# Optimization experiments

Hardware: AMD Instinct MI355X
Metric: run time of the kernel (lower is better)

Reference implementation:

```python
import jax, jax.numpy as jnp
import numpy as np

BATCH = 4096
DIM = 128
TEMP = 0.5
EPS = 1e-8


def _neg_mask(batch):
    n = 2 * batch
    m = np.ones((n, n), dtype=bool)
    np.fill_diagonal(m, False)
    idx = np.arange(batch)
    m[idx, idx + batch] = False
    m[idx + batch, idx] = False
    return m


def setup_inputs() -> dict:
    key = jax.random.key(0)
    k1, k2 = jax.random.split(key)
    zx = jax.random.normal(k1, (BATCH, DIM), dtype=jnp.float32)
    zy = jax.random.normal(k2, (BATCH, DIM), dtype=jnp.float32)
    return {"zx": zx, "zy": zy}


def reference(zx, zy):
    batch = zx.shape[0]
    n = 2 * batch  # N = 2 * batch_size
    z = jnp.concatenate([zx, zy], axis=0)  # [N, D]
    # cosine similarity = normalized GEMM (avoids O(N^2*D) intermediate)
    norm = jnp.maximum(jnp.linalg.norm(z, axis=1, keepdims=True), EPS)
    zn = z / norm
    sim = (zn @ zn.T) / TEMP  # [N, N]
    # positives: diagonals at offsets +batch and -batch
    sim_xy = jnp.diagonal(sim, offset=batch)
    sim_yx = jnp.diagonal(sim, offset=-batch)
    positives = jnp.concatenate([sim_xy, sim_yx]).reshape(n, 1)  # [N, 1]
    # negatives: mask out diagonal and positive pairs (static boolean mask)
    mask = _neg_mask(batch)
    negatives = sim[mask].reshape(n, n - 2)  # [N, N-2]
    logits = jnp.concatenate([positives, negatives], axis=1)  # [N, N-1]
    # CrossEntropy(labels=0, reduction='sum') / N
    loss = jnp.sum(jax.nn.logsumexp(logits, axis=1) - logits[:, 0]) / n
    return loss
```

## Files before the change

kernel.cpp:

```cpp
#include <hip/hip_runtime.h>
#include <hip/hip_bf16.h>

#define BATCH 4096
#define NROWS 8192
#define DIM   128
#define NTILE 64

typedef __bf16 bf16x8 __attribute__((ext_vector_type(8)));
typedef __bf16 bf16x2 __attribute__((ext_vector_type(2)));
typedef float  f32x4  __attribute__((ext_vector_type(4)));

typedef const __attribute__((address_space(1))) unsigned int* gptr_t;
typedef __attribute__((address_space(3))) unsigned int* lptr_t;

__global__ __launch_bounds__(256) void normalize_kernel(
    const float* __restrict__ zx, const float* __restrict__ zy,
    ushort* __restrict__ zn, float* __restrict__ S, float* __restrict__ out)
{
  const int tid  = threadIdx.x;
  const int lane = tid & 63;
  const int w    = tid >> 6;
  const int row  = blockIdx.x * 4 + w;
  if (blockIdx.x < 32) S[blockIdx.x * 256 + tid] = 0.f;
  if (blockIdx.x == 0 && tid == 0) out[0] = 0.f;
  const float* src = (row < BATCH) ? (zx + (size_t)row * DIM)
                                   : (zy + (size_t)(row - BATCH) * DIM);
  float2 v = ((const float2*)src)[lane];
  float ss = v.x * v.x + v.y * v.y;
#pragma unroll
  for (int off = 1; off < 64; off <<= 1)
    ss += __shfl_xor(ss, off, 64);
  float inv = 1.0f / fmaxf(sqrtf(ss), 1e-8f);
  bf16x2 st;
  st.x = (__bf16)(v.x * inv);
  st.y = (__bf16)(v.y * inv);
  reinterpret_cast<bf16x2*>(zn + (size_t)row * DIM)[lane] = st;
}

__global__ __launch_bounds__(256, 2) void simloss_kernel(
    const ushort* __restrict__ zn, float* __restrict__ S,
    float* __restrict__ P)
{
  __shared__ ushort Bs[2][128 * 128];
  const int tid  = threadIdx.x;
  const int lane = tid & 63;
  const int w    = tid >> 6;
  const int wr   = w >> 1, wc = w & 1;
  const int q    = lane >> 4;
  const int l15  = lane & 15;

  const int p  = blockIdx.x >> 4;
  const int ch = blockIdx.x & 15;
  const int o0 = (ch == 0) ? 0 : 1 + ch * 4;
  const int T  = (ch == 0) ? 5 : 4;
  const int L0 = p + 1;

  auto tile_rc = [&](int o, int& rb, int& cb) {
    if (o < L0) { rb = p;      cb = o; }
    else        { rb = 63 - p; cb = o - L0; }
  };

  auto stage = [&](int cb, int buf) {
    const int C0 = cb * 128;
#pragma unroll
    for (int j = 0; j < 8; ++j) {
      const int Lbase = w * 512 + j * 64;
      const int row   = w * 32 + j * 4 + q;
      const int c     = l15 ^ (row & 15);
      const ushort* g = zn + (size_t)(C0 + row) * DIM + c * 8;
      __builtin_amdgcn_global_load_lds((gptr_t)g, (lptr_t)(&Bs[buf][Lbase * 8]),
                                       16, 0, 0);
    }
  };

  bf16x8 af[4][4];
  auto loadA = [&](int rb) {
    const int arow = rb * 128 + wr * 64 + l15;
#pragma unroll
    for (int mi = 0; mi < 4; ++mi)
#pragma unroll
      for (int ks = 0; ks < 4; ++ks) {
        const ushort* ap = zn + (size_t)(arow + mi * 16) * DIM + ks * 32 + q * 8;
        af[mi][ks] = *reinterpret_cast<const bf16x8*>(ap);
      }
  };

  int rb0, cb0;
  tile_rc(o0, rb0, cb0);
  stage(cb0, 0);
  loadA(rb0);

  f32x4 Srow[4];
#pragma unroll
  for (int mi = 0; mi < 4; ++mi) Srow[mi] = (f32x4){0.f, 0.f, 0.f, 0.f};

  const float K1 = 2.8853900817779268f;

  __syncthreads();

  for (int t = 0; t < T; ++t) {
    const int o = o0 + t;
    int trb, tcb;
    tile_rc(o, trb, tcb);
    int nrb = -1, ncb = -1;
    if (t + 1 < T) {
      tile_rc(o + 1, nrb, ncb);
      stage(ncb, (t & 1) ^ 1);
    }

    const ushort* bsc = &Bs[t & 1][0];

    f32x4 acc[4][4];
#pragma unroll
    for (int mi = 0; mi < 4; ++mi)
#pragma unroll
      for (int ni = 0; ni < 4; ++ni)
        acc[mi][ni] = (f32x4){0.f, 0.f, 0.f, 0.f};

#pragma unroll
    for (int ks = 0; ks < 4; ++ks) {
      bf16x8 bf[4];
#pragma unroll
      for (int ni = 0; ni < 4; ++ni) {
        const int nl  = wc * 64 + ni * 16 + l15;
        const int ck  = ks * 4 + q;
        const int L   = nl * 16 + (ck ^ (nl & 15));
        bf[ni] = *reinterpret_cast<const bf16x8*>(bsc + L * 8);
      }
#pragma unroll
      for (int mi = 0; mi < 4; ++mi)
#pragma unroll
        for (int ni = 0; ni < 4; ++ni)
          acc[mi][ni] = __builtin_amdgcn_mfma_f32_16x16x32_bf16(
              af[mi][ks], bf[ni], acc[mi][ni], 0, 0, 0);
    }

    const bool diag = (trb == tcb);
    float Scol[4];
#pragma unroll
    for (int ni = 0; ni < 4; ++ni) Scol[ni] = 0.f;

#pragma unroll
    for (int mi = 0; mi < 4; ++mi)
#pragma unroll
      for (int ni = 0; ni < 4; ++ni) {
        f32x4 vv;
#pragma unroll
        for (int r = 0; r < 4; ++r) {
          float d = acc[mi][ni][r];
          float v = __builtin_amdgcn_exp2f(fmaf(d, K1, -K1));
          if (diag) {
            const int rl = wr * 64 + mi * 16 + q * 4 + r;
            const int cl = wc * 64 + ni * 16 + l15;
            if (rl == cl) v = 0.f;
          }
          vv[r] = v;
        }
        Srow[mi] += vv;
        Scol[ni] += (vv[0] + vv[1]) + (vv[2] + vv[3]);
      }

    if (trb - tcb == 32) {
#pragma unroll
      for (int mi = 0; mi < 4; ++mi) {
        const int rl0 = wr * 64 + mi * 16 + q * 4;
#pragma unroll
        for (int ni = 0; ni < 4; ++ni) {
          const int cl = wc * 64 + ni * 16 + l15;
#pragma unroll
          for (int r = 0; r < 4; ++r) {
            if (cl == rl0 + r) {
              const int gr = trb * 128 + rl0 + r;
              const float pv = 2.0f * acc[mi][ni][r];
              P[gr] = pv;
              P[gr - 4096] = pv;
            }
          }
        }
      }
    }

    if (!diag) {
#pragma unroll
      for (int ni = 0; ni < 4; ++ni) {
        float v = Scol[ni];
        v += __shfl_xor(v, 16, 64);
        v += __shfl_xor(v, 32, 64);
        if (lane < 16)
          atomicAdd(&S[tcb * 128 + wc * 64 + ni * 16 + l15], v);
      }
    }

    const bool flushR = (t == T - 1) || (nrb != trb);
    if (flushR) {
#pragma unroll
      for (int mi = 0; mi < 4; ++mi)
#pragma unroll
        for (int r = 0; r < 4; ++r) {
          float v = Srow[mi][r];
          v += __shfl_xor(v, 1, 64);
          v += __shfl_xor(v, 2, 64);
          v += __shfl_xor(v, 4, 64);
          v += __shfl_xor(v, 8, 64);
          if (l15 == 0)
            atomicAdd(&S[trb * 128 + wr * 64 + mi * 16 + q * 4 + r], v);
        }
#pragma unroll
      for (int mi = 0; mi < 4; ++mi) Srow[mi] = (f32x4){0.f, 0.f, 0.f, 0.f};
    }

    if (t + 1 < T) {
      if (nrb != trb) loadA(nrb);
      __syncthreads();
    }
  }
}

__global__ __launch_bounds__(256) void finalize_kernel(
    const float* __restrict__ S, const float* __restrict__ P,
    float* __restrict__ out)
{
  const int i = blockIdx.x * 256 + threadIdx.x;
  float c = 2.0f + logf(S[i]) - P[i];
#pragma unroll
  for (int off = 1; off < 64; off <<= 1)
    c += __shfl_xor(c, off, 64);
  __shared__ float wsum[4];
  const int lane = threadIdx.x & 63, w = threadIdx.x >> 6;
  if (lane == 0) wsum[w] = c;
  __syncthreads();
  if (threadIdx.x == 0)
    atomicAdd(out, (wsum[0] + wsum[1] + wsum[2] + wsum[3]) * (1.0f / NROWS));
}

extern "C" void kernel_launch(void* const* d_in, const int* in_sizes, int n_in,
                              void* d_out, int out_size, void* d_ws, size_t ws_size,
                              hipStream_t stream)
{
  const float* zx = (const float*)d_in[0];
  const float* zy = (const float*)d_in[1];
  ushort* zn = (ushort*)d_ws;
  float*  P  = (float*)((char*)d_ws + (size_t)NROWS * DIM * 2);
  float*  S  = P + NROWS;
  float*  out = (float*)d_out;

  normalize_kernel<<<NROWS / 4, 256, 0, stream>>>(zx, zy, zn, S, out);
  simloss_kernel<<<512, 256, 0, stream>>>(zn, S, P);
  finalize_kernel<<<NROWS / 256, 256, 0, stream>>>(S, P, out);
}
```

Before: 83.76 us.

## Drop LDS staging of B tiles, load B fragments directly from global, double grid

The simloss kernel no longer stages B tiles into shared memory with global_load_lds double buffering and barriers. Each wave now loads its B fragments straight from global memory (relying on L1/L2 caching), and the block-level syncthreads calls are removed. The grid doubles to 1024 blocks with 2-3 tiles each, and the occupancy hint rises to 3 blocks per SM. The aim is to remove LDS traffic and synchronisation and to improve latency hiding. The cost is redundant global/L2 loads across waves and less reuse of B per block.

```diff
diff --git a/kernel.cpp b/kernel.cpp
--- a/kernel.cpp
+++ b/kernel.cpp
@@ -9,9 +9,6 @@
 typedef __bf16 bf16x8 __attribute__((ext_vector_type(8)));
 typedef __bf16 bf16x2 __attribute__((ext_vector_type(2)));
 typedef float  f32x4  __attribute__((ext_vector_type(4)));
-
-typedef const __attribute__((address_space(1))) unsigned int* gptr_t;
-typedef __attribute__((address_space(3))) unsigned int* lptr_t;
 
 __global__ __launch_bounds__(256) void normalize_kernel(
     const float* __restrict__ zx, const float* __restrict__ zy,
@@ -37,11 +34,10 @@
   reinterpret_cast<bf16x2*>(zn + (size_t)row * DIM)[lane] = st;
 }
 
-__global__ __launch_bounds__(256, 2) void simloss_kernel(
+__global__ __launch_bounds__(256, 3) void simloss_kernel(
     const ushort* __restrict__ zn, float* __restrict__ S,
     float* __restrict__ P)
 {
-  __shared__ ushort Bs[2][128 * 128];
   const int tid  = threadIdx.x;
   const int lane = tid & 63;
   const int w    = tid >> 6;
@@ -49,10 +45,10 @@
   const int q    = lane >> 4;
   const int l15  = lane & 15;
 
-  const int p  = blockIdx.x >> 4;
-  const int ch = blockIdx.x & 15;
-  const int o0 = (ch == 0) ? 0 : 1 + ch * 4;
-  const int T  = (ch == 0) ? 5 : 4;
+  const int p  = blockIdx.x >> 5;
+  const int ch = blockIdx.x & 31;
+  const int o0 = (ch == 0) ? 0 : 1 + ch * 2;
+  const int T  = (ch == 0) ? 3 : 2;
   const int L0 = p + 1;
 
   auto tile_rc = [&](int o, int& rb, int& cb) {
@@ -60,19 +56,6 @@
     else        { rb = 63 - p; cb = o - L0; }
   };
 
-  auto stage = [&](int cb, int buf) {
-    const int C0 = cb * 128;
-#pragma unroll
-    for (int j = 0; j < 8; ++j) {
-      const int Lbase = w * 512 + j * 64;
-      const int row   = w * 32 + j * 4 + q;
-      const int c     = l15 ^ (row & 15);
-      const ushort* g = zn + (size_t)(C0 + row) * DIM + c * 8;
-      __builtin_amdgcn_global_load_lds((gptr_t)g, (lptr_t)(&Bs[buf][Lbase * 8]),
-                                       16, 0, 0);
-    }
-  };
-
   bf16x8 af[4][4];
   auto loadA = [&](int rb) {
     const int arow = rb * 128 + wr * 64 + l15;
@@ -87,7 +70,6 @@
 
   int rb0, cb0;
   tile_rc(o0, rb0, cb0);
-  stage(cb0, 0);
   loadA(rb0);
 
   f32x4 Srow[4];
@@ -95,20 +77,13 @@
   for (int mi = 0; mi < 4; ++mi) Srow[mi] = (f32x4){0.f, 0.f, 0.f, 0.f};
 
   const float K1 = 2.8853900817779268f;
-
-  __syncthreads();
 
   for (int t = 0; t < T; ++t) {
     const int o = o0 + t;
     int trb, tcb;
     tile_rc(o, trb, tcb);
     int nrb = -1, ncb = -1;
-    if (t + 1 < T) {
-      tile_rc(o + 1, nrb, ncb);
-      stage(ncb, (t & 1) ^ 1);
-    }
-
-    const ushort* bsc = &Bs[t & 1][0];
+    if (t + 1 < T) tile_rc(o + 1, nrb, ncb);
 
     f32x4 acc[4][4];
 #pragma unroll
@@ -117,15 +92,15 @@
       for (int ni = 0; ni < 4; ++ni)
         acc[mi][ni] = (f32x4){0.f, 0.f, 0.f, 0.f};
 
+    const ushort* bbase = zn + (size_t)(tcb * 128) * DIM;
 #pragma unroll
     for (int ks = 0; ks < 4; ++ks) {
       bf16x8 bf[4];
 #pragma unroll
       for (int ni = 0; ni < 4; ++ni) {
-        const int nl  = wc * 64 + ni * 16 + l15;
-        const int ck  = ks * 4 + q;
-        const int L   = nl * 16 + (ck ^ (nl & 15));
-        bf[ni] = *reinterpret_cast<const bf16x8*>(bsc + L * 8);
+        const int nl = wc * 64 + ni * 16 + l15;
+        bf[ni] = *reinterpret_cast<const bf16x8*>(
+            bbase + (size_t)nl * DIM + ks * 32 + q * 8);
       }
 #pragma unroll
       for (int mi = 0; mi < 4; ++mi)
@@ -207,11 +182,7 @@
         }
 #pragma unroll
       for (int mi = 0; mi < 4; ++mi) Srow[mi] = (f32x4){0.f, 0.f, 0.f, 0.f};
-    }
-
-    if (t + 1 < T) {
-      if (nrb != trb) loadA(nrb);
-      __syncthreads();
+      if (t + 1 < T && nrb != trb) loadA(nrb);
     }
   }
 }
@@ -245,6 +216,6 @@
   float*  out = (float*)d_out;
 
   normalize_kernel<<<NROWS / 4, 256, 0, stream>>>(zx, zy, zn, S, out);
-  simloss_kernel<<<512, 256, 0, stream>>>(zn, S, P);
+  simloss_kernel<<<1024, 256, 0, stream>>>(zn, S, P);
   finalize_kernel<<<NROWS / 256, 256, 0, stream>>>(S, P, out);
 }
```

Measured after the change: 127.8 us. 52.5% more time.

## Replace float atomics with per-slot partial-sum buffers reduced in finalize

Applied to the files above, without the earlier changes.

Each tile now writes its row and column exp-sums to a dedicated slot in a 128×8192 partial buffer, with plain stores instead of atomicAdd. The finalize kernel sums the 128 slots per row before taking the log. This removes atomic contention and the separate zeroing of S in the normalize kernel. In exchange, row sums are flushed after every tile, and finalize reads a 4 MB buffer using only 32 blocks.

```diff
diff --git a/kernel.cpp b/kernel.cpp
--- a/kernel.cpp
+++ b/kernel.cpp
@@ -5,6 +5,7 @@
 #define NROWS 8192
 #define DIM   128
 #define NTILE 64
+#define NSLOT 128
 
 typedef __bf16 bf16x8 __attribute__((ext_vector_type(8)));
 typedef __bf16 bf16x2 __attribute__((ext_vector_type(2)));
@@ -15,13 +16,12 @@
 
 __global__ __launch_bounds__(256) void normalize_kernel(
     const float* __restrict__ zx, const float* __restrict__ zy,
-    ushort* __restrict__ zn, float* __restrict__ S, float* __restrict__ out)
+    ushort* __restrict__ zn, float* __restrict__ out)
 {
   const int tid  = threadIdx.x;
   const int lane = tid & 63;
   const int w    = tid >> 6;
   const int row  = blockIdx.x * 4 + w;
-  if (blockIdx.x < 32) S[blockIdx.x * 256 + tid] = 0.f;
   if (blockIdx.x == 0 && tid == 0) out[0] = 0.f;
   const float* src = (row < BATCH) ? (zx + (size_t)row * DIM)
                                    : (zy + (size_t)(row - BATCH) * DIM);
@@ -38,7 +38,7 @@
 }
 
 __global__ __launch_bounds__(256, 2) void simloss_kernel(
-    const ushort* __restrict__ zn, float* __restrict__ S,
+    const ushort* __restrict__ zn, float* __restrict__ Spart,
     float* __restrict__ P)
 {
   __shared__ ushort Bs[2][128 * 128];
@@ -89,10 +89,6 @@
   tile_rc(o0, rb0, cb0);
   stage(cb0, 0);
   loadA(rb0);
-
-  f32x4 Srow[4];
-#pragma unroll
-  for (int mi = 0; mi < 4; ++mi) Srow[mi] = (f32x4){0.f, 0.f, 0.f, 0.f};
 
   const float K1 = 2.8853900817779268f;
 
@@ -136,7 +132,10 @@
     }
 
     const bool diag = (trb == tcb);
+    f32x4 Srow[4];
     float Scol[4];
+#pragma unroll
+    for (int mi = 0; mi < 4; ++mi) Srow[mi] = (f32x4){0.f, 0.f, 0.f, 0.f};
 #pragma unroll
     for (int ni = 0; ni < 4; ++ni) Scol[ni] = 0.f;
 
@@ -180,6 +179,24 @@
       }
     }
 
+#pragma unroll
+    for (int mi = 0; mi < 4; ++mi) {
+      f32x4 v = Srow[mi];
+#pragma unroll
+      for (int r = 0; r < 4; ++r) {
+        float s = v[r];
+        s += __shfl_xor(s, 1, 64);
+        s += __shfl_xor(s, 2, 64);
+        s += __shfl_xor(s, 4, 64);
+        s += __shfl_xor(s, 8, 64);
+        v[r] = s;
+      }
+      if (l15 == 0)
+        *reinterpret_cast<f32x4*>(
+            &Spart[(size_t)(tcb * 2 + wc) * NROWS +
+                   trb * 128 + wr * 64 + mi * 16 + q * 4]) = v;
+    }
+
     if (!diag) {
 #pragma unroll
       for (int ni = 0; ni < 4; ++ni) {
@@ -187,26 +204,9 @@
         v += __shfl_xor(v, 16, 64);
         v += __shfl_xor(v, 32, 64);
         if (lane < 16)
-          atomicAdd(&S[tcb * 128 + wc * 64 + ni * 16 + l15], v);
-      }
-    }
-
-    const bool flushR = (t == T - 1) || (nrb != trb);
-    if (flushR) {
-#pragma unroll
-      for (int mi = 0; mi < 4; ++mi)
-#pragma unroll
-        for (int r = 0; r < 4; ++r) {
-          float v = Srow[mi][r];
-          v += __shfl_xor(v, 1, 64);
-          v += __shfl_xor(v, 2, 64);
-          v += __shfl_xor(v, 4, 64);
-          v += __shfl_xor(v, 8, 64);
-          if (l15 == 0)
-            atomicAdd(&S[trb * 128 + wr * 64 + mi * 16 + q * 4 + r], v);
-        }
-#pragma unroll
-      for (int mi = 0; mi < 4; ++mi) Srow[mi] = (f32x4){0.f, 0.f, 0.f, 0.f};
+          Spart[(size_t)(trb * 2 + wr) * NROWS +
+                tcb * 128 + wc * 64 + ni * 16 + l15] = v;
+      }
     }
 
     if (t + 1 < T) {
@@ -217,11 +217,14 @@
 }
 
 __global__ __launch_bounds__(256) void finalize_kernel(
-    const float* __restrict__ S, const float* __restrict__ P,
+    const float* __restrict__ Spart, const float* __restrict__ P,
     float* __restrict__ out)
 {
   const int i = blockIdx.x * 256 + threadIdx.x;
-  float c = 2.0f + logf(S[i]) - P[i];
+  float s = 0.f;
+#pragma unroll 8
+  for (int k = 0; k < NSLOT; ++k) s += Spart[(size_t)k * NROWS + i];
+  float c = 2.0f + logf(s) - P[i];
 #pragma unroll
   for (int off = 1; off < 64; off <<= 1)
     c += __shfl_xor(c, off, 64);
@@ -241,10 +244,10 @@
   const float* zy = (const float*)d_in[1];
   ushort* zn = (ushort*)d_ws;
   float*  P  = (float*)((char*)d_ws + (size_t)NROWS * DIM * 2);
-  float*  S  = P + NROWS;
+  float*  Sp = P + NROWS;
   float*  out = (float*)d_out;
 
-  normalize_kernel<<<NROWS / 4, 256, 0, stream>>>(zx, zy, zn, S, out);
-  simloss_kernel<<<512, 256, 0, stream>>>(zn, S, P);
-  finalize_kernel<<<NROWS / 256, 256, 0, stream>>>(S, P, out);
-}
+  normalize_kernel<<<NROWS / 4, 256, 0, stream>>>(zx, zy, zn, out);
+  simloss_kernel<<<512, 256, 0, stream>>>(zn, Sp, P);
+  finalize_kernel<<<NROWS / 256, 256, 0, stream>>>(Sp, P, out);
+}
```

New measurement: 93.55 us. 11.7% more time.
